# Optimization experiments

Hardware: AMD Instinct MI355X
Metric: run time of the kernel (lower is better)

The kernel has to match this reference:

```python
import jax, jax.numpy as jnp
import numpy as np
from jax import lax

K = 2       # kernel_size
STRIDE = 2  # stride (== kernel_size by default)


def setup_inputs() -> dict:
    key = jax.random.key(0)
    k1, k2, k3 = jax.random.split(key, 3)
    x = jax.random.normal(k1, (16, 192, 224, 224), dtype=jnp.float32)
    w_avg = jax.random.uniform(k2, (1, 192, 1, 1), dtype=jnp.float32)
    w_max = jax.random.uniform(k3, (1, 192, 1, 1), dtype=jnp.float32)
    return {"x": x, "w_avg": w_avg, "w_max": w_max}


def reference(x, w_avg, w_max):
    # CombPool2d, coefficient_type='channelwise':
    #   out = (w_avg**2) * avg_pool(x) + (w_max**2) * max_pool(x)
    # Window over spatial dims of NCHW input; no padding, dilation=1.
    win = (1, 1, K, K)
    strides = (1, 1, STRIDE, STRIDE)
    avg = lax.reduce_window(x, 0.0, lax.add, win, strides, 'VALID') / (K * K)
    mx = lax.reduce_window(x, -jnp.inf, lax.max, win, strides, 'VALID')
    # coefficients (1,C,1,1) broadcast over (B,C,H',W')
    return (w_avg ** 2) * avg + (w_max ** 2) * mx
```

## Files before the change

kernel.cpp:

```cpp
#include <hip/hip_runtime.h>


#define IN_HW   (224 * 224)
#define OUT_HW  (112 * 112)
#define NCH     192

__global__ __launch_bounds__(256) void combpool2d_kernel(
    const float* __restrict__ x,
    const float* __restrict__ w_avg,
    const float* __restrict__ w_max,
    float* __restrict__ out,
    int n2)
{
    int i = blockIdx.x * blockDim.x + threadIdx.x;
    if (i >= n2) return;

    int ow2 = i % 56;
    int t   = i / 56;
    int oh  = t % 112;
    int bc  = t / 112;
    int c   = bc % NCH;

    const float* row0 = x + (size_t)bc * IN_HW + (size_t)(2 * oh) * 224;
    float4 a = ((const float4*)row0)[ow2];
    float4 b = ((const float4*)(row0 + 224))[ow2];

    float ca = w_avg[c]; ca *= ca;
    float cm = w_max[c]; cm *= cm;

    float avg0 = 0.25f * ((a.x + a.y) + (b.x + b.y));
    float mx0  = fmaxf(fmaxf(a.x, a.y), fmaxf(b.x, b.y));
    float avg1 = 0.25f * ((a.z + a.w) + (b.z + b.w));
    float mx1  = fmaxf(fmaxf(a.z, a.w), fmaxf(b.z, b.w));

    float2 o;
    o.x = ca * avg0 + cm * mx0;
    o.y = ca * avg1 + cm * mx1;

    float* orow = out + (size_t)bc * OUT_HW + (size_t)oh * 112;
    ((float2*)orow)[ow2] = o;
}

extern "C" void kernel_launch(void* const* d_in, const int* in_sizes, int n_in,
                              void* d_out, int out_size, void* d_ws, size_t ws_size,
                              hipStream_t stream) {
    const float* x     = (const float*)d_in[0];
    const float* w_avg = (const float*)d_in[1];
    const float* w_max = (const float*)d_in[2];
    float* out = (float*)d_out;

    int n2 = out_size / 2;
    int block = 256;
    int grid = (n2 + block - 1) / block;
    combpool2d_kernel<<<grid, block, 0, stream>>>(x, w_avg, w_max, out, n2);
}
```

Measured before the change: 808.5 us.

## Process four outputs per thread with nontemporal loads/stores and grid-stride loop

Each thread now produces four pooled outputs, reading two 16-byte vectors from each input row and writing one 16-byte vector. Loads and stores use nontemporal builtins to avoid polluting caches with streaming data. The launch is capped at 2048 blocks with a grid-stride loop. This reduces the number of memory instructions per output, but fewer threads in flight could lower memory-level parallelism.

```diff
diff --git a/kernel.cpp b/kernel.cpp
--- a/kernel.cpp
+++ b/kernel.cpp
@@ -1,5 +1,7 @@
 #include <hip/hip_runtime.h>
 
+
+typedef float f4 __attribute__((ext_vector_type(4)));
 
 #define IN_HW   (224 * 224)
 #define OUT_HW  (112 * 112)
@@ -10,35 +12,41 @@
     const float* __restrict__ w_avg,
     const float* __restrict__ w_max,
     float* __restrict__ out,
-    int n2)
+    int n4)
 {
-    int i = blockIdx.x * blockDim.x + threadIdx.x;
-    if (i >= n2) return;
+    int stride = gridDim.x * blockDim.x;
+    for (int i = blockIdx.x * blockDim.x + threadIdx.x; i < n4; i += stride) {
+        int ow4 = i % 28;
+        int t   = i / 28;
+        int oh  = t % 112;
+        int bc  = t / 112;
+        int c   = bc % NCH;
 
-    int ow2 = i % 56;
-    int t   = i / 56;
-    int oh  = t % 112;
-    int bc  = t / 112;
-    int c   = bc % NCH;
+        const float* row0 = x + (size_t)bc * IN_HW + (size_t)(2 * oh) * 224;
+        const f4* r0 = (const f4*)row0;
+        const f4* r1 = (const f4*)(row0 + 224);
 
-    const float* row0 = x + (size_t)bc * IN_HW + (size_t)(2 * oh) * 224;
-    float4 a = ((const float4*)row0)[ow2];
-    float4 b = ((const float4*)(row0 + 224))[ow2];
+        f4 a0 = __builtin_nontemporal_load(&r0[2 * ow4]);
+        f4 a1 = __builtin_nontemporal_load(&r0[2 * ow4 + 1]);
+        f4 b0 = __builtin_nontemporal_load(&r1[2 * ow4]);
+        f4 b1 = __builtin_nontemporal_load(&r1[2 * ow4 + 1]);
 
-    float ca = w_avg[c]; ca *= ca;
-    float cm = w_max[c]; cm *= cm;
+        float ca = w_avg[c]; ca *= ca;
+        float cm = w_max[c]; cm *= cm;
 
-    float avg0 = 0.25f * ((a.x + a.y) + (b.x + b.y));
-    float mx0  = fmaxf(fmaxf(a.x, a.y), fmaxf(b.x, b.y));
-    float avg1 = 0.25f * ((a.z + a.w) + (b.z + b.w));
-    float mx1  = fmaxf(fmaxf(a.z, a.w), fmaxf(b.z, b.w));
+        f4 o;
+        o.x = ca * (0.25f * ((a0.x + a0.y) + (b0.x + b0.y)))
+            + cm * fmaxf(fmaxf(a0.x, a0.y), fmaxf(b0.x, b0.y));
+        o.y = ca * (0.25f * ((a0.z + a0.w) + (b0.z + b0.w)))
+            + cm * fmaxf(fmaxf(a0.z, a0.w), fmaxf(b0.z, b0.w));
+        o.z = ca * (0.25f * ((a1.x + a1.y) + (b1.x + b1.y)))
+            + cm * fmaxf(fmaxf(a1.x, a1.y), fmaxf(b1.x, b1.y));
+        o.w = ca * (0.25f * ((a1.z + a1.w) + (b1.z + b1.w)))
+            + cm * fmaxf(fmaxf(a1.z, a1.w), fmaxf(b1.z, b1.w));
 
-    float2 o;
-    o.x = ca * avg0 + cm * mx0;
-    o.y = ca * avg1 + cm * mx1;
-
-    float* orow = out + (size_t)bc * OUT_HW + (size_t)oh * 112;
-    ((float2*)orow)[ow2] = o;
+        f4* orow = (f4*)(out + (size_t)bc * OUT_HW + (size_t)oh * 112);
+        __builtin_nontemporal_store(o, &orow[ow4]);
+    }
 }
 
 extern "C" void kernel_launch(void* const* d_in, const int* in_sizes, int n_in,
@@ -49,8 +57,9 @@
     const float* w_max = (const float*)d_in[2];
     float* out = (float*)d_out;
 
-    int n2 = out_size / 2;
+    int n4 = out_size / 4;
     int block = 256;
-    int grid = (n2 + block - 1) / block;
-    combpool2d_kernel<<<grid, block, 0, stream>>>(x, w_avg, w_max, out, n2);
+    int grid = (n4 + block - 1) / block;
+    if (grid > 2048) grid = 2048;
+    combpool2d_kernel<<<grid, block, 0, stream>>>(x, w_avg, w_max, out, n4);
 }
```

New measurement: 798.3 us. Within noise of the previous version (-1.3%).
